# Kernel optimization log

Measured on AMD Instinct MI355X. Metric: run time of the kernel, lower is better.

Reference implementation:

```python
import jax, jax.numpy as jnp
import numpy as np

C = 128
EPS = 1e-5

def setup_inputs() -> dict:
    key = jax.random.key(0)
    ks = jax.random.split(key, 12)
    B, D, H, W = 2, 16, 16, 16
    inp = jax.random.normal(ks[0], (B, C, D, H, W), dtype=jnp.float32)
    s = 1.0 / np.sqrt(C)
    return {
        "inp": inp,
        "gamma": jnp.ones((C,), jnp.float32),
        "beta": jnp.zeros((C,), jnp.float32),
        "Wq": jax.random.normal(ks[1], (C, C), jnp.float32) * s,
        "bq": jnp.zeros((C,), jnp.float32),
        "Wk": jax.random.normal(ks[2], (C, C), jnp.float32) * s,
        "bk": jnp.zeros((C,), jnp.float32),
        "Wv": jax.random.normal(ks[3], (C, C), jnp.float32) * s,
        "bv": jnp.zeros((C,), jnp.float32),
        "Wo": jax.random.normal(ks[4], (C, C), jnp.float32) * s,
        "bo": jnp.zeros((C,), jnp.float32),
    }

def reference(inp, gamma, beta, Wq, bq, Wk, bk, Wv, bv, Wo, bo):
    B, ch, D, H, W = inp.shape
    N = D * H * W
    x = inp.reshape(B, ch, N)  # (B,C,N)
    # BatchNorm3d (training-mode batch stats, biased variance, affine)
    mean = jnp.mean(x, axis=(0, 2))
    var = jnp.var(x, axis=(0, 2))
    hn = (x - mean[None, :, None]) * jax.lax.rsqrt(var + EPS)[None, :, None]
    hn = hn * gamma[None, :, None] + beta[None, :, None]
    # 1x1 Conv3d == per-voxel channel mixing
    q = jnp.einsum('oc,bcn->bon', Wq, hn) + bq[None, :, None]
    k = jnp.einsum('oc,bcn->bon', Wk, hn) + bk[None, :, None]
    v = jnp.einsum('oc,bcn->bon', Wv, hn) + bv[None, :, None]
    scale = 1.0 / jnp.sqrt(jnp.asarray(ch, q.dtype))
    # attn[b,i,j] = softmax_j( q_i . k_j / sqrt(C) )
    attn = jax.nn.softmax(jnp.einsum('bci,bcj->bij', q, k) * scale, axis=-1)
    # out[b,c,i] = sum_j v[b,c,j] * attn[b,i,j]
    h = jnp.einsum('bcj,bij->bci', v, attn)
    h = jnp.einsum('oc,bcn->bon', Wo, h) + bo[None, :, None]
    return inp + h.reshape(B, ch, D, H, W)
```

## Files before the change

kernel.cpp:

```cpp
#include <hip/hip_runtime.h>

#define C 128
#define NSP 4096
#define BB 2
#define EPS 1e-5f

typedef float f32x4 __attribute__((ext_vector_type(4)));
typedef __bf16 bf16x8 __attribute__((ext_vector_type(8)));
typedef __bf16 bf16x4 __attribute__((ext_vector_type(4)));

__device__ __forceinline__ float b2f(__bf16 x) { return (float)x; }
__device__ __forceinline__ __bf16 f2b(float x) { return (__bf16)x; }

__device__ __forceinline__ float fexp2(float x) {
#if __has_builtin(__builtin_amdgcn_exp2f)
    return __builtin_amdgcn_exp2f(x);
#else
    return exp2f(x);
#endif
}

__device__ __forceinline__ bool is_bf(const void* gamma) {
    return *(const unsigned int*)gamma == 0x3F803F80u;
}
__device__ __forceinline__ float ldf(const void* p, size_t i, bool bf) {
    return bf ? (float)((const __bf16*)p)[i] : ((const float*)p)[i];
}
struct F8 { float v[8]; };
__device__ __forceinline__ F8 ld8(const void* p, size_t i, bool bf) {
    F8 r;
    if (bf) {
        bf16x8 t = *(const bf16x8*)((const __bf16*)p + i);
#pragma unroll
        for (int k = 0; k < 8; k++) r.v[k] = (float)t[k];
    } else {
        const float4* q = (const float4*)((const float*)p + i);
        float4 a = q[0], b = q[1];
        r.v[0]=a.x; r.v[1]=a.y; r.v[2]=a.z; r.v[3]=a.w;
        r.v[4]=b.x; r.v[5]=b.y; r.v[6]=b.z; r.v[7]=b.w;
    }
    return r;
}

__device__ __forceinline__ void cp16(const void* g, void* l) {
    __builtin_amdgcn_global_load_lds(
        (const __attribute__((address_space(1))) unsigned int*)g,
        (__attribute__((address_space(3))) unsigned int*)l, 16, 0, 0);
}

__global__ void k_stats(const void* __restrict__ x, const void* __restrict__ gamma,
                        float* __restrict__ meanv, float* __restrict__ rstd) {
    bool bf = is_bf(gamma);
    int c = blockIdx.x;
    int tid = threadIdx.x;
    float s = 0.f, ss = 0.f;
#pragma unroll
    for (int it = 0; it < 4; it++) {
        int flat = tid + it * 256;
        int half = flat >> 9;
        size_t off = ((size_t)(half * C + c)) * NSP + (size_t)(flat & 511) * 8;
        F8 v = ld8(x, off, bf);
#pragma unroll
        for (int k = 0; k < 8; k++) { s += v.v[k]; ss += v.v[k] * v.v[k]; }
    }
    for (int d = 32; d; d >>= 1) { s += __shfl_down(s, d); ss += __shfl_down(ss, d); }
    __shared__ float sh[8];
    int wv = tid >> 6, ln = tid & 63;
    if (ln == 0) { sh[wv] = s; sh[4 + wv] = ss; }
    __syncthreads();
    if (tid == 0) {
        float S = sh[0] + sh[1] + sh[2] + sh[3];
        float SS = sh[4] + sh[5] + sh[6] + sh[7];
        float m = S / (float)(BB * NSP);
        float v = SS / (float)(BB * NSP) - m * m;
        meanv[c] = m;
        rstd[c] = rsqrtf(fmaxf(v, 0.f) + EPS);
    }
}

__global__ void k_fold(const void* __restrict__ Wq, const void* __restrict__ bq,
                       const void* __restrict__ Wk, const void* __restrict__ bk,
                       const void* __restrict__ Wv, const void* __restrict__ bv,
                       const void* __restrict__ gamma, const void* __restrict__ beta,
                       const float* __restrict__ meanv, const float* __restrict__ rstd,
                       __bf16* __restrict__ Wp, float* __restrict__ bp) {
    bool bfm = is_bf(gamma);
    int o = blockIdx.x;
    int m = blockIdx.y;
    int c = threadIdx.x;
    const void* W  = (m == 0) ? Wq : ((m == 1) ? Wk : Wv);
    const void* bi = (m == 0) ? bq : ((m == 1) ? bk : bv);
    float scl = (m == 0) ? (0.08838834764831845f * 1.4426950408889634f) : 1.0f;
    float w = ldf(W, (size_t)o * C + c, bfm);
    float g = ldf(gamma, c, bfm) * rstd[c];
    Wp[((size_t)m * C + o) * C + c] = f2b(w * g * scl);
    float contrib = w * (ldf(beta, c, bfm) - g * meanv[c]);
    for (int d = 32; d; d >>= 1) contrib += __shfl_down(contrib, d);
    __shared__ float sh[2];
    if ((c & 63) == 0) sh[c >> 6] = contrib;
    __syncthreads();
    if (c == 0) bp[m * C + o] = (ldf(bi, o, bfm) + sh[0] + sh[1]) * scl;
}

__global__ void k_qkv(const void* __restrict__ x, const __bf16* __restrict__ Wp,
                      const float* __restrict__ bp, const void* __restrict__ gamma,
                      __bf16* __restrict__ Qt, __bf16* __restrict__ Kt,
                      __bf16* __restrict__ Vn) {
    bool bf = is_bf(gamma);
    __shared__ __attribute__((aligned(16))) __bf16 wsh[C * 136];
    __shared__ __attribute__((aligned(16))) __bf16 xsh[C * 72];
    __shared__ float bsh[C];
    int b = blockIdx.z, m = blockIdx.y, nt = blockIdx.x * 64;
    int tid = threadIdx.x;
    const __bf16* W = Wp + (size_t)m * C * C;
#pragma unroll
    for (int it = 0; it < 8; it++) {
        int flat = tid + it * 256;
        int o = flat >> 4, c0 = (flat & 15) * 8;
        *(bf16x8*)(wsh + o * 136 + c0) = *(const bf16x8*)(W + (size_t)o * C + c0);
    }
    size_t xbase = (size_t)b * C * NSP;
#pragma unroll
    for (int it = 0; it < 4; it++) {
        int flat = tid + it * 256;
        int c = flat >> 3, nc = (flat & 7) * 8;
        F8 v = ld8(x, xbase + (size_t)c * NSP + nt + nc, bf);
        bf16x8 tv;
#pragma unroll
        for (int k = 0; k < 8; k++) tv[k] = f2b(v.v[k]);
        *(bf16x8*)(xsh + c * 72 + nc) = tv;
    }
    if (tid < C) bsh[tid] = bp[m * C + tid];
    __syncthreads();

    int o0 = (tid >> 4) * 8;
    int n0 = (tid & 15) * 4;
    float acc[8][4];
#pragma unroll
    for (int i = 0; i < 8; i++) {
        float bias = bsh[o0 + i];
#pragma unroll
        for (int k = 0; k < 4; k++) acc[i][k] = bias;
    }
    for (int c = 0; c < C; c += 4) {
        float xf[4][4];
#pragma unroll
        for (int cc = 0; cc < 4; cc++) {
            bf16x4 x4 = *(const bf16x4*)(xsh + (c + cc) * 72 + n0);
#pragma unroll
            for (int k = 0; k < 4; k++) xf[cc][k] = b2f(x4[k]);
        }
#pragma unroll
        for (int i = 0; i < 8; i++) {
            bf16x4 w4 = *(const bf16x4*)(wsh + (o0 + i) * 136 + c);
#pragma unroll
            for (int cc = 0; cc < 4; cc++) {
                float wf = b2f(w4[cc]);
#pragma unroll
                for (int k = 0; k < 4; k++) acc[i][k] += wf * xf[cc][k];
            }
        }
    }
    if (m < 2) {
        __bf16* base = ((m == 0) ? Qt : Kt) + ((size_t)b * NSP + nt + n0) * C + o0;
#pragma unroll
        for (int k = 0; k < 4; k++) {
            bf16x8 tv;
#pragma unroll
            for (int i = 0; i < 8; i++) tv[i] = f2b(acc[i][k]);
            *(bf16x8*)(base + (size_t)k * C) = tv;
        }
    } else {
#pragma unroll
        for (int i = 0; i < 8; i++) {
            bf16x4 tv;
#pragma unroll
            for (int k = 0; k < 4; k++) tv[k] = f2b(acc[i][k]);
            *(bf16x4*)(Vn + ((size_t)b * C + o0 + i) * NSP + nt + n0) = tv;
        }
    }
}

#define KT_OFF(buf) ((buf) * 32768)
#define VT_OFF(buf) (65536 + (buf) * 32768)
#define PT_OFF      131072
#define LSH_OFF     139264

__launch_bounds__(512, 2)
__global__ void k_attn(const __bf16* __restrict__ Qt, const __bf16* __restrict__ Kt,
                       const __bf16* __restrict__ Vn, const void* __restrict__ gamma,
                       const void* __restrict__ Wo, const void* __restrict__ bo,
                       const void* __restrict__ inp,
                       void* __restrict__ Oc ) {
    extern __shared__ char smem[];
    __bf16* pt = (__bf16*)(smem + PT_OFF);
    float* lsh = (float*)(smem + LSH_OFF);

    bool bf = is_bf(gamma);
    int qt = blockIdx.x, b = blockIdx.y;
    int tid = threadIdx.x;
    int w = tid >> 6, lane = tid & 63, quad = lane >> 4, l15 = lane & 15;
    int s = w & 3, h = w >> 2;

    const __bf16* kb = Kt + (size_t)b * NSP * C;
    const __bf16* vb = Vn + (size_t)b * C * NSP;

    bf16x8 qreg[2][4];
#pragma unroll
    for (int it2 = 0; it2 < 2; it2++)
#pragma unroll
        for (int ks = 0; ks < 4; ks++)
            qreg[it2][ks] = *(const bf16x8*)(Qt + ((size_t)b * NSP + qt * 32 + it2 * 16 + l15) * C + ks * 32 + quad * 8);

    auto stageK = [&](int tile, int buf) {
        __bf16* kt = (__bf16*)(smem + KT_OFF(buf));
#pragma unroll
        for (int c4 = 0; c4 < 4; c4++) {
            int ch = w * 4 + c4;
            int jl = ch * 4 + (lane >> 4);
            int p = lane & 15;
            int cb = p ^ (jl & 15);
            cp16(kb + ((size_t)(tile * 128 + jl)) * C + cb * 8, kt + ch * 512);
        }
    };
    auto stageV = [&](int tile, int buf) {
        __bf16* vt = (__bf16*)(smem + VT_OFF(buf));
#pragma unroll
        for (int c4 = 0; c4 < 4; c4++) {
            int ch = w * 4 + c4;
            int cl = ch * 4 + (lane >> 4);
            int p = lane & 15;
            int jc = p ^ (cl & 15);
            cp16(vb + (size_t)cl * NSP + tile * 128 + jc * 8, vt + ch * 512);
        }
    };

    f32x4 o_acc[4][2];
#pragma unroll
    for (int cb2 = 0; cb2 < 4; cb2++)
#pragma unroll
        for (int it2 = 0; it2 < 2; it2++)
            o_acc[cb2][it2] = (f32x4){0.f, 0.f, 0.f, 0.f};
    float l_acc[2] = {0.f, 0.f};

    stageK(0, 0); stageV(0, 0);

#pragma unroll 2
    for (int it = 0; it < 32; it++) {
        int cur = it & 1, nxt = cur ^ 1;
        const __bf16* ktc = (const __bf16*)(smem + KT_OFF(cur));
        const __bf16* vtc = (const __bf16*)(smem + VT_OFF(cur));
        asm volatile("s_waitcnt vmcnt(4) lgkmcnt(0)\n\ts_barrier" ::: "memory");
        if (it < 31) stageK(it + 1, nxt);
        f32x4 sacc[2];
        sacc[0] = (f32x4){0.f, 0.f, 0.f, 0.f};
        sacc[1] = (f32x4){0.f, 0.f, 0.f, 0.f};
#pragma unroll
        for (int ks = 0; ks < 4; ks++) {
            bf16x8 kf = *(const bf16x8*)(ktc + (w * 16 + l15) * 128 + (((ks * 4 + quad) ^ l15) * 8));
            sacc[0] = __builtin_amdgcn_mfma_f32_16x16x32_bf16(kf, qreg[0][ks], sacc[0], 0, 0, 0);
            sacc[1] = __builtin_amdgcn_mfma_f32_16x16x32_bf16(kf, qreg[1][ks], sacc[1], 0, 0, 0);
        }
#pragma unroll
        for (int it2 = 0; it2 < 2; it2++) {
            bf16x4 p4;
#pragma unroll
            for (int r = 0; r < 4; r++) {
                float p = fexp2(sacc[it2][r]);
                l_acc[it2] += p;
                p4[r] = f2b(p);
            }
            int i = it2 * 16 + l15;
            int cc = 2 * w + (quad >> 1);
            *(bf16x4*)(pt + i * 128 + ((cc ^ (i & 7)) * 8) + (quad & 1) * 4) = p4;
        }
        if (it < 31) {
            asm volatile("s_waitcnt vmcnt(4) lgkmcnt(0)\n\ts_barrier" ::: "memory");
            stageV(it + 1, nxt);
        } else {
            asm volatile("s_waitcnt vmcnt(0) lgkmcnt(0)\n\ts_barrier" ::: "memory");
        }
        bf16x8 pfr[2];
#pragma unroll
        for (int it2 = 0; it2 < 2; it2++) {
            int i = it2 * 16 + l15;
            pfr[it2] = *(const bf16x8*)(pt + i * 128 + (((s * 4 + quad) ^ (i & 7)) * 8));
        }
#pragma unroll
        for (int cblk = 0; cblk < 4; cblk++) {
            bf16x8 vf = *(const bf16x8*)(vtc + (h * 64 + cblk * 16 + l15) * 128 + (((s * 4 + quad) ^ l15) * 8));
            o_acc[cblk][0] = __builtin_amdgcn_mfma_f32_16x16x32_bf16(vf, pfr[0], o_acc[cblk][0], 0, 0, 0);
            o_acc[cblk][1] = __builtin_amdgcn_mfma_f32_16x16x32_bf16(vf, pfr[1], o_acc[cblk][1], 0, 0, 0);
        }
    }

#pragma unroll
    for (int it2 = 0; it2 < 2; it2++) {
        l_acc[it2] += __shfl_xor(l_acc[it2], 16);
        l_acc[it2] += __shfl_xor(l_acc[it2], 32);
    }
    if (lane < 16) { lsh[w * 32 + lane] = l_acc[0]; lsh[w * 32 + 16 + lane] = l_acc[1]; }
    float* arrf = (float*)smem;
#pragma unroll
    for (int cblk = 0; cblk < 4; cblk++)
#pragma unroll
        for (int it2 = 0; it2 < 2; it2++)
#pragma unroll
            for (int r = 0; r < 4; r++)
                arrf[(s * 128 + h * 64 + cblk * 16 + quad * 4 + r) * 37 + it2 * 16 + l15] = o_acc[cblk][it2][r];
    __syncthreads();
    if (tid < 32) {
        float ls = 0.f;
#pragma unroll
        for (int w8 = 0; w8 < 8; w8++) ls += lsh[w8 * 32 + tid];
        lsh[256 + tid] = 1.0f / ls;
    }
    __syncthreads();
    __bf16* osh = (__bf16*)(smem + VT_OFF(1));
    {
        int i = tid >> 4, c0 = (tid & 15) * 8;
        float rl = lsh[256 + i];
        bf16x8 tv;
#pragma unroll
        for (int k = 0; k < 8; k++) {
            int c = c0 + k;
            float v = arrf[(0 * 128 + c) * 37 + i] + arrf[(1 * 128 + c) * 37 + i]
                    + arrf[(2 * 128 + c) * 37 + i] + arrf[(3 * 128 + c) * 37 + i];
            tv[k] = f2b(v * rl);
        }
        *(bf16x8*)(osh + i * 136 + c0) = tv;
    }
    __syncthreads();
    __bf16* wsh = (__bf16*)smem;
    float* bsh = (float*)(smem + PT_OFF);
#pragma unroll
    for (int it4 = 0; it4 < 4; it4++) {
        int flat = tid + it4 * 512;
        int o = flat >> 4, c0 = (flat & 15) * 8;
        F8 v = ld8(Wo, (size_t)o * C + c0, bf);
        bf16x8 tv;
#pragma unroll
        for (int k = 0; k < 8; k++) tv[k] = f2b(v.v[k]);
        *(bf16x8*)(wsh + o * 136 + c0) = tv;
    }
    if (tid < C) bsh[tid] = ldf(bo, tid, bf);
    __syncthreads();
    f32x4 pacc[2];
    pacc[0] = (f32x4){0.f, 0.f, 0.f, 0.f};
    pacc[1] = (f32x4){0.f, 0.f, 0.f, 0.f};
#pragma unroll
    for (int ks = 0; ks < 4; ks++) {
        bf16x8 wf  = *(const bf16x8*)(wsh + (w * 16 + l15) * 136 + (ks * 4 + quad) * 8);
        bf16x8 of0 = *(const bf16x8*)(osh + (0 * 16 + l15) * 136 + (ks * 4 + quad) * 8);
        bf16x8 of1 = *(const bf16x8*)(osh + (1 * 16 + l15) * 136 + (ks * 4 + quad) * 8);
        pacc[0] = __builtin_amdgcn_mfma_f32_16x16x32_bf16(wf, of0, pacc[0], 0, 0, 0);
        pacc[1] = __builtin_amdgcn_mfma_f32_16x16x32_bf16(wf, of1, pacc[1], 0, 0, 0);
    }
#pragma unroll
    for (int it2 = 0; it2 < 2; it2++)
#pragma unroll
        for (int r = 0; r < 4; r++) {
            int o = w * 16 + quad * 4 + r;
            int i = it2 * 16 + l15;
            size_t addr = ((size_t)b * C + o) * NSP + qt * 32 + i;
            float val = pacc[it2][r] + bsh[o] + ldf(inp, addr, bf);
            if (bf) ((__bf16*)Oc)[addr] = f2b(val);
            else    ((float*)Oc)[addr] = val;
        }
}

extern "C" void kernel_launch(void* const* d_in, const int* in_sizes, int n_in,
                              void* d_out, int out_size, void* d_ws, size_t ws_size,
                              hipStream_t stream) {
    const void* inp   = d_in[0];
    const void* gamma = d_in[1];
    const void* beta  = d_in[2];
    const void* Wq    = d_in[3];
    const void* bq    = d_in[4];
    const void* Wk    = d_in[5];
    const void* bk    = d_in[6];
    const void* Wv    = d_in[7];
    const void* bv    = d_in[8];
    const void* Wo    = d_in[9];
    const void* bo    = d_in[10];

    char* ws = (char*)d_ws;
    float* meanv = (float*)(ws + 0);
    float* rstd  = (float*)(ws + 512);
    float* bp    = (float*)(ws + 1024);
    __bf16* Wp = (__bf16*)(ws + 4096);
    __bf16* Qt = (__bf16*)(ws + 131072);
    __bf16* Kt = (__bf16*)(ws + 2228224);
    __bf16* Vn = (__bf16*)(ws + 4325376);

    (void)hipFuncSetAttribute((const void*)k_attn,
                              hipFuncAttributeMaxDynamicSharedMemorySize, 140416);

    k_stats<<<dim3(C), dim3(256), 0, stream>>>(inp, gamma, meanv, rstd);
    k_fold<<<dim3(C, 3), dim3(C), 0, stream>>>(Wq, bq, Wk, bk, Wv, bv, gamma, beta, meanv, rstd, Wp, bp);
    k_qkv<<<dim3(64, 3, 2), dim3(256), 0, stream>>>(inp, Wp, bp, gamma, Qt, Kt, Vn);
    k_attn<<<dim3(128, 2), dim3(512), 140416, stream>>>(Qt, Kt, Vn, gamma, Wo, bo, inp, d_out);
}
```

Baseline: 131.3 us.

## Use MFMA bf16 matrix instructions for the QKV projection kernel

Replaces the scalar FMA loop in the QKV 1x1-conv projection with 16x16x32 bf16 MFMA instructions. Weight fragments are loaded straight into registers, and the input tile is staged as fp32, then transposed into a swizzled bf16 layout in shared memory to feed the MFMA operands. For V the operand order is swapped so stores stay contiguous along the spatial axis. This cuts ALU work in the projection, but it adds an extra shared-memory pass and sync, and the projection is a small part of total time next to attention.

```diff
diff --git a/kernel.cpp b/kernel.cpp
--- a/kernel.cpp
+++ b/kernel.cpp
@@ -102,81 +102,86 @@
     if (c == 0) bp[m * C + o] = (ldf(bi, o, bfm) + sh[0] + sh[1]) * scl;
 }
 
+__launch_bounds__(256)
 __global__ void k_qkv(const void* __restrict__ x, const __bf16* __restrict__ Wp,
                       const float* __restrict__ bp, const void* __restrict__ gamma,
                       __bf16* __restrict__ Qt, __bf16* __restrict__ Kt,
                       __bf16* __restrict__ Vn) {
     bool bf = is_bf(gamma);
-    __shared__ __attribute__((aligned(16))) __bf16 wsh[C * 136];
-    __shared__ __attribute__((aligned(16))) __bf16 xsh[C * 72];
+    __shared__ __attribute__((aligned(16))) float xf[C * 68];
+    __shared__ __attribute__((aligned(16))) __bf16 xbf[64 * C];
     __shared__ float bsh[C];
     int b = blockIdx.z, m = blockIdx.y, nt = blockIdx.x * 64;
     int tid = threadIdx.x;
+    int w = tid >> 6, lane = tid & 63, quad = lane >> 4, l15 = lane & 15;
     const __bf16* W = Wp + (size_t)m * C * C;
-#pragma unroll
-    for (int it = 0; it < 8; it++) {
-        int flat = tid + it * 256;
-        int o = flat >> 4, c0 = (flat & 15) * 8;
-        *(bf16x8*)(wsh + o * 136 + c0) = *(const bf16x8*)(W + (size_t)o * C + c0);
-    }
+
+    bf16x8 wfrag[2][4];
+#pragma unroll
+    for (int ot = 0; ot < 2; ot++)
+#pragma unroll
+        for (int ks = 0; ks < 4; ks++)
+            wfrag[ot][ks] = *(const bf16x8*)(W + (size_t)(w * 32 + ot * 16 + l15) * C + (ks * 4 + quad) * 8);
+
     size_t xbase = (size_t)b * C * NSP;
 #pragma unroll
     for (int it = 0; it < 4; it++) {
         int flat = tid + it * 256;
         int c = flat >> 3, nc = (flat & 7) * 8;
         F8 v = ld8(x, xbase + (size_t)c * NSP + nt + nc, bf);
-        bf16x8 tv;
-#pragma unroll
-        for (int k = 0; k < 8; k++) tv[k] = f2b(v.v[k]);
-        *(bf16x8*)(xsh + c * 72 + nc) = tv;
+        float4 t0, t1;
+        t0.x = v.v[0]; t0.y = v.v[1]; t0.z = v.v[2]; t0.w = v.v[3];
+        t1.x = v.v[4]; t1.y = v.v[5]; t1.z = v.v[6]; t1.w = v.v[7];
+        *(float4*)(xf + c * 68 + nc) = t0;
+        *(float4*)(xf + c * 68 + nc + 4) = t1;
     }
     if (tid < C) bsh[tid] = bp[m * C + tid];
     __syncthreads();
-
-    int o0 = (tid >> 4) * 8;
-    int n0 = (tid & 15) * 4;
-    float acc[8][4];
-#pragma unroll
-    for (int i = 0; i < 8; i++) {
-        float bias = bsh[o0 + i];
-#pragma unroll
-        for (int k = 0; k < 4; k++) acc[i][k] = bias;
-    }
-    for (int c = 0; c < C; c += 4) {
-        float xf[4][4];
-#pragma unroll
-        for (int cc = 0; cc < 4; cc++) {
-            bf16x4 x4 = *(const bf16x4*)(xsh + (c + cc) * 72 + n0);
-#pragma unroll
-            for (int k = 0; k < 4; k++) xf[cc][k] = b2f(x4[k]);
-        }
-#pragma unroll
-        for (int i = 0; i < 8; i++) {
-            bf16x4 w4 = *(const bf16x4*)(wsh + (o0 + i) * 136 + c);
-#pragma unroll
-            for (int cc = 0; cc < 4; cc++) {
-                float wf = b2f(w4[cc]);
-#pragma unroll
-                for (int k = 0; k < 4; k++) acc[i][k] += wf * xf[cc][k];
+    {
+        int n = tid & 63, cg = tid >> 6;
+#pragma unroll
+        for (int s4 = 0; s4 < 4; s4++) {
+            int cc = cg * 4 + s4;
+            bf16x8 tv;
+#pragma unroll
+            for (int k = 0; k < 8; k++) tv[k] = f2b(xf[(cc * 8 + k) * 68 + n]);
+            *(bf16x8*)(xbf + n * C + ((cc ^ (n & 15)) * 8)) = tv;
+        }
+    }
+    __syncthreads();
+
+#pragma unroll
+    for (int nt2 = 0; nt2 < 4; nt2++) {
+        bf16x8 xfrag[4];
+        int n = nt2 * 16 + l15;
+#pragma unroll
+        for (int ks = 0; ks < 4; ks++)
+            xfrag[ks] = *(const bf16x8*)(xbf + n * C + (((ks * 4 + quad) ^ (n & 15)) * 8));
+#pragma unroll
+        for (int ot = 0; ot < 2; ot++) {
+            f32x4 acc = (f32x4){0.f, 0.f, 0.f, 0.f};
+            if (m < 2) {
+#pragma unroll
+                for (int ks = 0; ks < 4; ks++)
+                    acc = __builtin_amdgcn_mfma_f32_16x16x32_bf16(wfrag[ot][ks], xfrag[ks], acc, 0, 0, 0);
+                int o0 = w * 32 + ot * 16 + quad * 4;
+                int nn = nt + nt2 * 16 + l15;
+                bf16x4 tv;
+#pragma unroll
+                for (int r = 0; r < 4; r++) tv[r] = f2b(acc[r] + bsh[o0 + r]);
+                *(bf16x4*)(((m == 0) ? Qt : Kt) + ((size_t)b * NSP + nn) * C + o0) = tv;
+            } else {
+#pragma unroll
+                for (int ks = 0; ks < 4; ks++)
+                    acc = __builtin_amdgcn_mfma_f32_16x16x32_bf16(xfrag[ks], wfrag[ot][ks], acc, 0, 0, 0);
+                int n0 = nt + nt2 * 16 + quad * 4;
+                int o = w * 32 + ot * 16 + l15;
+                float bias = bsh[o];
+                bf16x4 tv;
+#pragma unroll
+                for (int r = 0; r < 4; r++) tv[r] = f2b(acc[r] + bias);
+                *(bf16x4*)(Vn + ((size_t)b * C + o) * NSP + n0) = tv;
             }
-        }
-    }
-    if (m < 2) {
-        __bf16* base = ((m == 0) ? Qt : Kt) + ((size_t)b * NSP + nt + n0) * C + o0;
-#pragma unroll
-        for (int k = 0; k < 4; k++) {
-            bf16x8 tv;
-#pragma unroll
-            for (int i = 0; i < 8; i++) tv[i] = f2b(acc[i][k]);
-            *(bf16x8*)(base + (size_t)k * C) = tv;
-        }
-    } else {
-#pragma unroll
-        for (int i = 0; i < 8; i++) {
-            bf16x4 tv;
-#pragma unroll
-            for (int k = 0; k < 4; k++) tv[k] = f2b(acc[i][k]);
-            *(bf16x4*)(Vn + ((size_t)b * C + o0 + i) * NSP + nt + n0) = tv;
         }
     }
 }
```

Result: faster. 119.6 us, median of 2 (-8.9%).
